# Optimization experiments

Measured on AMD Instinct MI355X. Metric: run time of the kernel, lower is better.

The kernel has to match this reference:

```python
import jax, jax.numpy as jnp
import numpy as np

D_MODEL = 1024
D_INNER = 2048  # expand * d_model
D_STATE = 16
D_CONV = 4
DT_RANK = 64    # ceil(d_model / 16)
B_SZ, L_SEQ = 2, 1024


def setup_inputs() -> dict:
    key = jax.random.key(0)
    ks = jax.random.split(key, 8)
    s = lambda fan_in: 1.0 / np.sqrt(fan_in)
    x = jax.random.normal(ks[0], (B_SZ, L_SEQ, D_MODEL), dtype=jnp.float32)
    in_proj_w = jax.random.normal(ks[1], (2 * D_INNER, D_MODEL), jnp.float32) * s(D_MODEL)
    conv_w = jax.random.normal(ks[2], (D_INNER, 1, D_CONV), jnp.float32) * s(D_CONV)
    conv_b = jax.random.normal(ks[3], (D_INNER,), jnp.float32) * 0.02
    x_proj_w = jax.random.normal(ks[4], (DT_RANK + 2 * D_STATE, D_INNER), jnp.float32) * s(D_INNER)
    dt_proj_w = jax.random.normal(ks[5], (D_INNER, DT_RANK), jnp.float32) * s(DT_RANK)
    dt_proj_b = jax.random.normal(ks[6], (D_INNER,), jnp.float32) * 0.02
    A_log = jnp.broadcast_to(jnp.log(jnp.arange(1, D_STATE + 1, dtype=jnp.float32)), (D_INNER, D_STATE))
    D_param = jnp.ones((D_INNER,), jnp.float32)
    out_proj_w = jax.random.normal(ks[7], (D_MODEL, D_INNER), jnp.float32) * s(D_INNER)
    return dict(x=x, in_proj_w=in_proj_w, conv_w=conv_w, conv_b=conv_b,
                x_proj_w=x_proj_w, dt_proj_w=dt_proj_w, dt_proj_b=dt_proj_b,
                A_log=A_log, D_param=D_param, out_proj_w=out_proj_w)


def _mamba_forward(x, in_proj_w, conv_w, conv_b, x_proj_w, dt_proj_w, dt_proj_b, A_log, D_param, out_proj_w):
    B, L, _ = x.shape
    # in_proj: (B,L,2*d_inner) -> split into conv branch and gate
    xz = jnp.einsum('bld,ed->ble', x, in_proj_w)
    x_br, z = jnp.split(xz, 2, axis=-1)
    # depthwise causal conv1d (left pad d_conv-1, truncate to L == torch pad+slice)
    xc = jnp.transpose(x_br, (0, 2, 1))  # (B, d_inner, L)
    xc = jax.lax.conv_general_dilated(
        xc, conv_w, window_strides=(1,), padding=[(D_CONV - 1, 0)],
        dimension_numbers=('NCH', 'OIH', 'NCH'), feature_group_count=D_INNER)
    xc = xc + conv_b[None, :, None]
    u = jax.nn.silu(jnp.transpose(xc, (0, 2, 1)))  # (B, L, d_inner) = SSM input
    # input-dependent params
    proj = jnp.einsum('bld,ed->ble', u, x_proj_w)
    delta_raw, B_in, C_in = jnp.split(proj, [DT_RANK, DT_RANK + D_STATE], axis=-1)
    delta = jax.nn.softplus(jnp.einsum('blr,dr->bld', delta_raw, dt_proj_w) + dt_proj_b)
    A = -jnp.exp(A_log)  # (d_inner, d_state)

    def step(h, inp):
        d_t, b_t, c_t, u_t = inp  # (B,d_inner),(B,d_state),(B,d_state),(B,d_inner)
        dA = jnp.exp(d_t[:, :, None] * A)                       # (B,d_inner,d_state)
        h = dA * h + (d_t * u_t)[:, :, None] * b_t[:, None, :]  # ZOH-ish update
        y_t = jnp.einsum('bds,bs->bd', h, c_t) + D_param * u_t
        return h, y_t

    h0 = jnp.zeros((B, D_INNER, D_STATE), dtype=x.dtype)
    inputs = (jnp.swapaxes(delta, 0, 1), jnp.swapaxes(B_in, 0, 1),
              jnp.swapaxes(C_in, 0, 1), jnp.swapaxes(u, 0, 1))
    _, ys = jax.lax.scan(step, h0, inputs)  # (L, B, d_inner)
    y = jnp.swapaxes(ys, 0, 1) * jax.nn.silu(z)
    return jnp.einsum('ble,de->bld', y, out_proj_w)


def reference(x, in_proj_w, conv_w, conv_b, x_proj_w, dt_proj_w, dt_proj_b, A_log, D_param, out_proj_w):
    return _mamba_forward(x, in_proj_w, conv_w, conv_b, x_proj_w, dt_proj_w, dt_proj_b, A_log, D_param, out_proj_w)
```

## Files before the change

kernel.cpp:

```cpp
#include <hip/hip_runtime.h>
#include <hip/hip_bf16.h>

#define D_MODEL 1024
#define D_INNER 2048
#define D_STATE 16
#define D_CONV  4
#define DT_RANK 64
#define B_SZ    2
#define L_SEQ   1024
#define BL      (B_SZ * L_SEQ)
#define NPROJ   (DT_RANK + 2 * D_STATE)

typedef __attribute__((ext_vector_type(8))) short bf16x8;
typedef __attribute__((ext_vector_type(4))) float floatx4;
typedef unsigned short ushort_t;

__device__ __forceinline__ void mfma_bf16(floatx4& acc, bf16x8 a, bf16x8 b) {
    asm volatile("v_mfma_f32_16x16x32_bf16 %0, %1, %2, %0"
                 : "+v"(acc) : "v"(a), "v"(b));
}

__device__ __forceinline__ void cvt_hilo(float f, ushort_t& hi, ushort_t& lo) {
    __hip_bfloat16 h = __float2bfloat16(f);
    hi = *(ushort_t*)&h;
    __hip_bfloat16 l = __float2bfloat16(f - __bfloat162float(h));
    lo = *(ushort_t*)&l;
}

__device__ __forceinline__ void cvt_store4(float4 v, ushort_t* hi, ushort_t* lo) {
    ushort4 h, l;
    cvt_hilo(v.x, h.x, l.x);
    cvt_hilo(v.y, h.y, l.y);
    cvt_hilo(v.z, h.z, l.z);
    cvt_hilo(v.w, h.w, l.w);
    *(ushort4*)hi = h;
    *(ushort4*)lo = l;
}

#define N4_WI 1048576
#define N4_WO 524288
#define N4_X  524288
#define N4_WD 32768
#define N4_TOT  (N4_WI + N4_WO + N4_X + N4_WD)

__global__ __launch_bounds__(256) void cvt_static(
    const float* __restrict__ wi, ushort_t* wihi, ushort_t* wilo,
    const float* __restrict__ wo, ushort_t* wohi, ushort_t* wolo,
    const float* __restrict__ x,  ushort_t* xhi,  ushort_t* xlo,
    const float* __restrict__ wd, ushort_t* wdhi, ushort_t* wdlo)
{
    int i = blockIdx.x * 256 + threadIdx.x;
    if (i >= N4_TOT) return;
    const float* src; ushort_t *dh, *dl;
    if (i < N4_WI)                 { src = wi; dh = wihi; dl = wilo; }
    else if ((i -= N4_WI) < N4_WO) { src = wo; dh = wohi; dl = wolo; }
    else if ((i -= N4_WO) < N4_X)  { src = x;  dh = xhi;  dl = xlo;  }
    else                           { i -= N4_X; src = wd; dh = wdhi; dl = wdlo; }
    float4 v = ((const float4*)src)[i];
    cvt_store4(v, dh + i * 4, dl + i * 4);
}

template <int TM, int TN, int KSPLIT, int EPI>
__global__ __launch_bounds__(256, 2) void gemm_pre(
    const ushort_t* __restrict__ Ahi, const ushort_t* __restrict__ Alo, int lda,
    const ushort_t* __restrict__ Bhi, const ushort_t* __restrict__ Blo, int ldb,
    float* __restrict__ C, int ldc, int K, size_t cslice,
    const float* __restrict__ bias)
{
    static_assert(TM == 128 && TN == 128, "stage mapping assumes 128x128");
    constexpr int LDT = 32;
    constexpr int IT = TM / 32, JT = TN / 32;
    __shared__ __align__(16) ushort_t As[2][2][TM * LDT];
    __shared__ __align__(16) ushort_t Bs[2][2][TN * LDT];

    const int tid = threadIdx.x;
    const int bm = blockIdx.y * TM;
    const int bn = blockIdx.x * TN;
    const int kstart = (KSPLIT > 1) ? blockIdx.z * (K / KSPLIT) : 0;
    const int kend   = (KSPLIT > 1) ? kstart + K / KSPLIT : K;

    const int wave = tid >> 6;
    const int lane = tid & 63;
    const int wm = (wave >> 1) * (TM / 2);
    const int wn = (wave & 1) * (TN / 2);
    const int ml = lane & 15;
    const int q  = lane >> 4;

    const ushort_t* gplane = (wave == 0) ? Ahi : (wave == 1) ? Alo
                           : (wave == 2) ? Bhi : Blo;
    const int grow0 = (wave < 2) ? bm : bn;
    const int gld   = (wave < 2) ? lda : ldb;
    const int rsub  = lane >> 2;
    const int gg    = ((lane & 3) ^ ((lane >> 3) & 3)) * 8;

    auto stage = [&](int buf, int kc) {
        ushort_t* lbase = (wave < 2) ? &As[buf][wave & 1][0]
                                     : &Bs[buf][wave & 1][0];
#pragma unroll
        for (int u = 0; u < 8; ++u) {
            const int R0 = u * 16;
            const ushort_t* src =
                gplane + (size_t)(grow0 + R0 + rsub) * gld + kc + gg;
            __builtin_amdgcn_global_load_lds(
                (const __attribute__((address_space(1))) unsigned int*)src,
                (__attribute__((address_space(3))) unsigned int*)(lbase + R0 * LDT),
                16, 0, 0);
        }
    };

    floatx4 acc[IT][JT];
#pragma unroll
    for (int i = 0; i < IT; ++i)
#pragma unroll
        for (int j = 0; j < JT; ++j) acc[i][j] = (floatx4)0.f;

    const int nt = (kend - kstart) >> 5;

    stage(0, kstart);
    __syncthreads();

    for (int t = 0; t < nt; ++t) {
        const int buf = t & 1;
        if (t + 1 < nt) stage(buf ^ 1, kstart + ((t + 1) << 5));

        bf16x8 ah[IT], al[IT], bh[JT], bl[JT];
#pragma unroll
        for (int i = 0; i < IT; ++i) {
            const int r = wm + i * 16 + ml;
            const int p = (q ^ ((r >> 1) & 3)) * 8;
            ah[i] = *(const bf16x8*)&As[buf][0][r * LDT + p];
            al[i] = *(const bf16x8*)&As[buf][1][r * LDT + p];
        }
#pragma unroll
        for (int j = 0; j < JT; ++j) {
            const int r = wn + j * 16 + ml;
            const int p = (q ^ ((r >> 1) & 3)) * 8;
            bh[j] = *(const bf16x8*)&Bs[buf][0][r * LDT + p];
            bl[j] = *(const bf16x8*)&Bs[buf][1][r * LDT + p];
        }
#pragma unroll
        for (int i = 0; i < IT; ++i)
#pragma unroll
            for (int j = 0; j < JT; ++j) {
                mfma_bf16(acc[i][j], ah[i], bh[j]);
                mfma_bf16(acc[i][j], ah[i], bl[j]);
                mfma_bf16(acc[i][j], al[i], bh[j]);
            }

        __syncthreads();
    }

    asm volatile("s_nop 7\n\ts_nop 7\n\ts_nop 7" ::: "memory");

    float* Cb = (KSPLIT > 1) ? C + (size_t)blockIdx.z * cslice : C;
#pragma unroll
    for (int i = 0; i < IT; ++i)
#pragma unroll
        for (int j = 0; j < JT; ++j) {
            const int col = bn + wn + j * 16 + ml;
            const float bv = (EPI == 1) ? bias[col] : 0.f;
#pragma unroll
            for (int r = 0; r < 4; ++r) {
                const int row = bm + wm + i * 16 + q * 4 + r;
                float v = acc[i][j][r];
                if (EPI == 1) {
                    v += bv;
                    v = (v > 20.f) ? v : log1pf(__expf(v));
                }
                Cb[(size_t)row * ldc + col] = v;
            }
        }
}

__global__ __launch_bounds__(256) void fold_out(
    const float* __restrict__ s, float* __restrict__ out)
{
    const int i = blockIdx.x * 256 + threadIdx.x;
    const float4* s4 = (const float4*)s;
    constexpr int SL = BL * D_MODEL / 4;
    float4 a = s4[i], b = s4[i + SL], c = s4[i + 2 * SL], d = s4[i + 3 * SL];
    ((float4*)out)[i] = make_float4(a.x + b.x + c.x + d.x,
                                    a.y + b.y + c.y + d.y,
                                    a.z + b.z + c.z + d.z,
                                    a.w + b.w + c.w + d.w);
}

__global__ __launch_bounds__(256) void fold_proj(
    const float* __restrict__ pp, float* __restrict__ proj,
    ushort_t* __restrict__ Phi, ushort_t* __restrict__ Plo)
{
    const int i = blockIdx.x * 256 + threadIdx.x;
    constexpr int SL = BL * NPROJ / 4;
    float4 acc = make_float4(0.f, 0.f, 0.f, 0.f);
#pragma unroll
    for (int sp = 0; sp < 16; ++sp) {
        float4 v = ((const float4*)pp)[i + sp * SL];
        acc.x += v.x; acc.y += v.y; acc.z += v.z; acc.w += v.w;
    }
    ((float4*)proj)[i] = acc;

    const int row = i / (NPROJ / 4);
    const int c4  = i % (NPROJ / 4);
    if (c4 < DT_RANK / 4)
        cvt_store4(acc, Phi + (size_t)row * DT_RANK + c4 * 4,
                        Plo + (size_t)row * DT_RANK + c4 * 4);
}

#define PKC 128
#define PSC 64

__global__ __launch_bounds__(256) void gemm_proj_conv(
    const float* __restrict__ xz,
    const float* __restrict__ conv_w,
    const float* __restrict__ conv_b,
    const float* __restrict__ Wp,
    float* __restrict__ projp,
    float* __restrict__ u_out)
{
    __shared__ float us[PSC][65];
    __shared__ float wsh[PSC][100];

    const int tid = threadIdx.x;
    const int bm = blockIdx.y * 64;
    const int kbase0 = blockIdx.x * PKC;

    const int tx = tid & 15;
    const int ty = tid >> 4;

    float acc[4][6];
#pragma unroll
    for (int i = 0; i < 4; ++i)
#pragma unroll
        for (int j = 0; j < 6; ++j) acc[i][j] = 0.f;

    for (int sc = 0; sc < PKC / PSC; ++sc) {
        const int kb = kbase0 + sc * PSC;
        __syncthreads();
#pragma unroll
        for (int i = 0; i < 4; ++i) {
            const int flat = tid + 256 * i;
            const int r  = flat >> 4;
            const int kk = (flat & 15) * 4;
            const int k  = kb + kk;
            const int rr = bm + r;
            const int t  = rr & (L_SEQ - 1);
            const float* base = xz + (size_t)rr * 4096 + k;
            float4 x0 = *(const float4*)(base);
            float4 x1 = (t >= 1) ? *(const float4*)(base - 4096)  : make_float4(0,0,0,0);
            float4 x2 = (t >= 2) ? *(const float4*)(base - 8192)  : make_float4(0,0,0,0);
            float4 x3 = (t >= 3) ? *(const float4*)(base - 12288) : make_float4(0,0,0,0);
            float4 cb = *(const float4*)(conv_b + k);
            float4 w0 = ((const float4*)conv_w)[k + 0];
            float4 w1 = ((const float4*)conv_w)[k + 1];
            float4 w2 = ((const float4*)conv_w)[k + 2];
            float4 w3 = ((const float4*)conv_w)[k + 3];
            float4 uo;
            { float a = cb.x + w0.x*x3.x + w0.y*x2.x + w0.z*x1.x + w0.w*x0.x;
              uo.x = a / (1.f + __expf(-a)); }
            { float a = cb.y + w1.x*x3.y + w1.y*x2.y + w1.z*x1.y + w1.w*x0.y;
              uo.y = a / (1.f + __expf(-a)); }
            { float a = cb.z + w2.x*x3.z + w2.y*x2.z + w2.z*x1.z + w2.w*x0.z;
              uo.z = a / (1.f + __expf(-a)); }
            { float a = cb.w + w3.x*x3.w + w3.y*x2.w + w3.z*x1.w + w3.w*x0.w;
              uo.w = a / (1.f + __expf(-a)); }
            us[kk + 0][r] = uo.x;
            us[kk + 1][r] = uo.y;
            us[kk + 2][r] = uo.z;
            us[kk + 3][r] = uo.w;
            *(float4*)(u_out + (size_t)rr * D_INNER + k) = uo;
        }
#pragma unroll
        for (int i = 0; i < 6; ++i) {
            const int flat = tid + 256 * i;
            const int r = flat >> 4;
            const int k4 = flat & 15;
            float4 v = *(const float4*)(Wp + (size_t)r * D_INNER + kb + k4 * 4);
            wsh[k4*4+0][r] = v.x; wsh[k4*4+1][r] = v.y;
            wsh[k4*4+2][r] = v.z; wsh[k4*4+3][r] = v.w;
        }
        __syncthreads();

#pragma unroll 8
        for (int kk = 0; kk < PSC; ++kk) {
            float a[4], b[6];
#pragma unroll
            for (int i = 0; i < 4; ++i) a[i] = us[kk][ty * 4 + i];
#pragma unroll
            for (int j = 0; j < 6; ++j) b[j] = wsh[kk][tx + 16 * j];
#pragma unroll
            for (int i = 0; i < 4; ++i)
#pragma unroll
                for (int j = 0; j < 6; ++j) acc[i][j] += a[i] * b[j];
        }
    }

    float* pb = projp + (size_t)blockIdx.x * (BL * NPROJ);
#pragma unroll
    for (int i = 0; i < 4; ++i)
#pragma unroll
        for (int j = 0; j < 6; ++j)
            pb[(size_t)(bm + ty * 4 + i) * NPROJ + tx + 16 * j] = acc[i][j];
}

template <int CSv>
__global__ __launch_bounds__(256) void scan_phase_a(
    const float* __restrict__ xz,
    const float* __restrict__ u,
    const float* __restrict__ proj,
    const float* __restrict__ A_log,
    float* __restrict__ hloc,
    float* __restrict__ sumd,
    int nc)
{
    const int d = blockIdx.x * 256 + threadIdx.x;
    const int c = blockIdx.y;
    const int b = blockIdx.z;

    float a[D_STATE];
#pragma unroll
    for (int s = 0; s < D_STATE; ++s) a[s] = -__expf(A_log[d * D_STATE + s]);

    float h[D_STATE];
#pragma unroll
    for (int s = 0; s < D_STATE; ++s) h[s] = 0.f;
    float sd = 0.f;

    for (int t = c * CSv; t < (c + 1) * CSv; ++t) {
        const size_t bt = (size_t)b * L_SEQ + t;
        const float dv = xz[bt * (2 * D_INNER) + d];
        const float uv = u[bt * D_INNER + d];
        const float du = dv * uv;
        sd += dv;
        const float* pr = proj + bt * NPROJ;
#pragma unroll
        for (int s = 0; s < D_STATE; ++s)
            h[s] = __expf(dv * a[s]) * h[s] + du * pr[DT_RANK + s];
    }

    const size_t base = ((size_t)(b * nc + c) * D_STATE) * D_INNER + d;
#pragma unroll
    for (int s = 0; s < D_STATE; ++s) hloc[base + (size_t)s * D_INNER] = h[s];
    sumd[(size_t)(b * nc + c) * D_INNER + d] = sd;
}

__global__ __launch_bounds__(256) void scan_phase_b(
    const float* __restrict__ hloc,
    const float* __restrict__ sumd,
    const float* __restrict__ A_log,
    float* __restrict__ carry,
    int nc)
{
    const int g = blockIdx.x * 256 + threadIdx.x;
    const int d = g & (D_INNER - 1);
    const int s = (g >> 11) & (D_STATE - 1);
    const int b = g >> 15;

    const float a_s = -__expf(A_log[d * D_STATE + s]);

    float hc = 0.f;
    carry[((size_t)(b * nc + 0) * D_STATE + s) * D_INNER + d] = 0.f;

    for (int c = 1; c < nc; ++c) {
        const float sd = sumd[(size_t)(b * nc + c - 1) * D_INNER + d];
        const float hl = hloc[((size_t)(b * nc + c - 1) * D_STATE + s) * D_INNER + d];
        hc = __expf(a_s * sd) * hc + hl;
        carry[((size_t)(b * nc + c) * D_STATE + s) * D_INNER + d] = hc;
    }
}

template <int CSv>
__global__ __launch_bounds__(256) void scan_phase_c(
    const float* __restrict__ xz,
    const float* __restrict__ u,
    const float* __restrict__ proj,
    const float* __restrict__ A_log,
    const float* __restrict__ D_param,
    const float* __restrict__ carry,
    ushort_t* __restrict__ Yhi,
    ushort_t* __restrict__ Ylo,
    int nc)
{
    const int d = blockIdx.x * 256 + threadIdx.x;
    const int c = blockIdx.y;
    const int b = blockIdx.z;

    float a[D_STATE];
#pragma unroll
    for (int s = 0; s < D_STATE; ++s) a[s] = -__expf(A_log[d * D_STATE + s]);
    const float Dp = D_param[d];

    float h[D_STATE];
    const size_t cbase = ((size_t)(b * nc + c) * D_STATE) * D_INNER + d;
#pragma unroll
    for (int s = 0; s < D_STATE; ++s) h[s] = carry[cbase + (size_t)s * D_INNER];

    for (int t = c * CSv; t < (c + 1) * CSv; ++t) {
        const size_t bt = (size_t)b * L_SEQ + t;
        const float dv = xz[bt * (2 * D_INNER) + d];
        const float uv = u[bt * D_INNER + d];
        const float du = dv * uv;
        const float* pr = proj + bt * NPROJ;

        float acc = 0.f;
#pragma unroll
        for (int s = 0; s < D_STATE; ++s) {
            h[s] = __expf(dv * a[s]) * h[s] + du * pr[DT_RANK + s];
            acc += h[s] * pr[DT_RANK + D_STATE + s];
        }
        const float yv = acc + Dp * uv;

        const float zv = xz[bt * (2 * D_INNER) + D_INNER + d];
        const float gate = zv / (1.f + __expf(-zv));
        ushort_t hh, ll;
        cvt_hilo(yv * gate, hh, ll);
        Yhi[bt * D_INNER + d] = hh;
        Ylo[bt * D_INNER + d] = ll;
    }
}

extern "C" void kernel_launch(void* const* d_in, const int* in_sizes, int n_in,
                              void* d_out, int out_size, void* d_ws, size_t ws_size,
                              hipStream_t stream)
{
    const float* x         = (const float*)d_in[0];
    const float* in_proj_w = (const float*)d_in[1];
    const float* conv_w    = (const float*)d_in[2];
    const float* conv_b    = (const float*)d_in[3];
    const float* x_proj_w  = (const float*)d_in[4];
    const float* dt_proj_w = (const float*)d_in[5];
    const float* dt_proj_b = (const float*)d_in[6];
    const float* A_log     = (const float*)d_in[7];
    const float* D_param   = (const float*)d_in[8];
    const float* out_proj_w= (const float*)d_in[9];
    float* out = (float*)d_out;

    const size_t fixed =
        (size_t)BL * 4096 * 4 +
        (size_t)BL * 2048 * 4 +
        (size_t)BL * NPROJ * 4 +
        (size_t)(4096 + 2048) * 1024 * 2 * 2;
    const size_t need64 = fixed + (size_t)B_SZ * 64 * D_INNER * 4
                                + (size_t)B_SZ * 64 * D_STATE * D_INNER * 4;
    const int nc = (ws_size >= need64) ? 64 : 32;
    const int cs = L_SEQ / nc;

    float* xz    = (float*)d_ws;
    float* u     = xz    + (size_t)BL * 4096;
    float* proj  = u     + (size_t)BL * 2048;
    float* sumd  = proj  + (size_t)BL * NPROJ;
    float* carry = sumd  + (size_t)B_SZ * nc * D_INNER;
    ushort_t* Wihi = (ushort_t*)(carry + (size_t)B_SZ * nc * D_STATE * D_INNER);
    ushort_t* Wilo = Wihi + (size_t)4096 * 1024;
    ushort_t* Wohi = Wilo + (size_t)4096 * 1024;
    ushort_t* Wolo = Wohi + (size_t)1024 * 2048;
    ushort_t* Xhi  = (ushort_t*)carry;
    ushort_t* Xlo  = Xhi + (size_t)BL * D_MODEL;
    float*    hloc = (float*)Wihi;
    ushort_t* Yhi  = Wihi;
    ushort_t* Ylo  = Wilo;
    float*    projp = (float*)Wihi;
    ushort_t* Phi  = Xhi;
    ushort_t* Plo  = Xhi + (size_t)BL * DT_RANK;
    ushort_t* Wdhi = (ushort_t*)sumd;
    ushort_t* Wdlo = Wdhi + (size_t)D_INNER * DT_RANK;
    float*    Cslc  = xz;

    dim3 blk(256);

    cvt_static<<<(N4_TOT + 255) / 256, blk, 0, stream>>>(
        in_proj_w, Wihi, Wilo, out_proj_w, Wohi, Wolo, x, Xhi, Xlo,
        dt_proj_w, Wdhi, Wdlo);

    gemm_pre<128, 128, 1, 0><<<dim3(4096 / 128, BL / 128), blk, 0, stream>>>(
        Xhi, Xlo, D_MODEL, Wihi, Wilo, D_MODEL, xz, 2 * D_INNER, D_MODEL, 0,
        nullptr);

    gemm_proj_conv<<<dim3(D_INNER / PKC, BL / 64), blk, 0, stream>>>(
        xz, conv_w, conv_b, x_proj_w, projp, u);

    fold_proj<<<(BL * NPROJ / 4) / 256, blk, 0, stream>>>(projp, proj, Phi, Plo);

    gemm_pre<128, 128, 1, 1><<<dim3(D_INNER / 128, BL / 128), blk, 0, stream>>>(
        Phi, Plo, DT_RANK, Wdhi, Wdlo, DT_RANK, xz, 2 * D_INNER, DT_RANK, 0,
        dt_proj_b);

    if (cs == 16) {
        scan_phase_a<16><<<dim3(D_INNER / 256, nc, B_SZ), blk, 0, stream>>>(
            xz, u, proj, A_log, hloc, sumd, nc);
    } else {
        scan_phase_a<32><<<dim3(D_INNER / 256, nc, B_SZ), blk, 0, stream>>>(
            xz, u, proj, A_log, hloc, sumd, nc);
    }
    scan_phase_b<<<dim3((B_SZ * D_INNER * D_STATE) / 256), blk, 0, stream>>>(
        hloc, sumd, A_log, carry, nc);
    if (cs == 16) {
        scan_phase_c<16><<<dim3(D_INNER / 256, nc, B_SZ), blk, 0, stream>>>(
            xz, u, proj, A_log, D_param, carry, Yhi, Ylo, nc);
    } else {
        scan_phase_c<32><<<dim3(D_INNER / 256, nc, B_SZ), blk, 0, stream>>>(
            xz, u, proj, A_log, D_param, carry, Yhi, Ylo, nc);
    }

    gemm_pre<128, 128, 4, 0><<<dim3(D_MODEL / 128, BL / 128, 4), blk, 0, stream>>>(
        Yhi, Ylo, D_INNER, Wohi, Wolo, D_INNER, Cslc, D_MODEL, D_INNER,
        (size_t)BL * D_MODEL, nullptr);
    fold_out<<<(BL * D_MODEL / 4) / 256, blk, 0, stream>>>(Cslc, out);
}
```

Baseline: 302.0 us.

## Add 512-thread 128x256 triple-buffered GEMM for in_proj and out_proj

Introduces a gemm_big kernel with 8 waves, a 128x256 output tile and a three-stage LDS ring. Six waves issue direct global-to-LDS loads and synchronisation uses vmcnt waits plus a raw s_barrier, so loads run two tiles ahead of compute. The in_proj and split-K out_proj GEMMs now use it, while gemm_pre keeps only the dt_proj path. The larger tile raises per-block data reuse and the deeper pipeline hides load latency, but it costs more LDS and registers (one block per CU) and leaves fewer blocks in each grid.

```diff
diff --git a/kernel.cpp b/kernel.cpp
--- a/kernel.cpp
+++ b/kernel.cpp
@@ -60,11 +60,120 @@
     cvt_store4(v, dh + i * 4, dl + i * 4);
 }
 
-template <int TM, int TN, int KSPLIT, int EPI>
+template <int KSPLIT>
+__global__ __launch_bounds__(512, 1) void gemm_big(
+    const ushort_t* __restrict__ Ahi, const ushort_t* __restrict__ Alo, int lda,
+    const ushort_t* __restrict__ Bhi, const ushort_t* __restrict__ Blo, int ldb,
+    float* __restrict__ C, int ldc, int K, size_t cslice)
+{
+    constexpr int BM = 128, BN = 256, LDT = 32;
+    __shared__ __align__(16) ushort_t As[3][2][BM * LDT];
+    __shared__ __align__(16) ushort_t Bs[3][2][BN * LDT];
+
+    const int tid = threadIdx.x;
+    const int bm = blockIdx.y * BM;
+    const int bn = blockIdx.x * BN;
+    const int kstart = (KSPLIT > 1) ? blockIdx.z * (K / KSPLIT) : 0;
+    const int nt = ((KSPLIT > 1) ? K / KSPLIT : K) >> 5;
+
+    const int wave = tid >> 6;
+    const int lane = tid & 63;
+    const int wm = (wave >> 2) * 64;
+    const int wn = (wave & 3) * 64;
+    const int ml = lane & 15;
+    const int q  = lane >> 4;
+
+    const int rsub = lane >> 2;
+    const int gg   = ((lane & 3) ^ ((lane >> 3) & 3)) * 8;
+    const ushort_t* gsrc = Ahi; int grow0 = bm, gld = lda;
+    if (wave == 1)      { gsrc = Alo; grow0 = bm;       gld = lda; }
+    else if (wave == 2) { gsrc = Bhi; grow0 = bn;       gld = ldb; }
+    else if (wave == 3) { gsrc = Bhi; grow0 = bn + 128; gld = ldb; }
+    else if (wave == 4) { gsrc = Blo; grow0 = bn;       gld = ldb; }
+    else if (wave == 5) { gsrc = Blo; grow0 = bn + 128; gld = ldb; }
+    const bool do_stage = (wave < 6);
+
+    auto stage = [&](int buf, int kc) {
+        if (!do_stage) return;
+        ushort_t* lb;
+        if (wave == 0)      lb = &As[buf][0][0];
+        else if (wave == 1) lb = &As[buf][1][0];
+        else if (wave == 2) lb = &Bs[buf][0][0];
+        else if (wave == 3) lb = &Bs[buf][0][128 * LDT];
+        else if (wave == 4) lb = &Bs[buf][1][0];
+        else                lb = &Bs[buf][1][128 * LDT];
+#pragma unroll
+        for (int u2 = 0; u2 < 8; ++u2) {
+            const int R0 = u2 * 16;
+            const ushort_t* src =
+                gsrc + (size_t)(grow0 + R0 + rsub) * gld + kc + gg;
+            __builtin_amdgcn_global_load_lds(
+                (const __attribute__((address_space(1))) unsigned int*)src,
+                (__attribute__((address_space(3))) unsigned int*)(lb + R0 * LDT),
+                16, 0, 0);
+        }
+    };
+
+    floatx4 acc[4][4];
+#pragma unroll
+    for (int i = 0; i < 4; ++i)
+#pragma unroll
+        for (int j = 0; j < 4; ++j) acc[i][j] = (floatx4)0.f;
+
+    stage(0, kstart);
+    if (nt > 1) stage(1, kstart + 32);
+
+    for (int t = 0; t < nt; ++t) {
+        asm volatile("s_waitcnt vmcnt(8)" ::: "memory");
+        __builtin_amdgcn_s_barrier();
+        if (t + 2 < nt) stage((t + 2) % 3, kstart + ((t + 2) << 5));
+
+        const int buf = t % 3;
+        bf16x8 ah[4], al[4], bh[4], bl[4];
+#pragma unroll
+        for (int i = 0; i < 4; ++i) {
+            const int r = wm + i * 16 + ml;
+            const int p = (q ^ ((r >> 1) & 3)) * 8;
+            ah[i] = *(const bf16x8*)&As[buf][0][r * LDT + p];
+            al[i] = *(const bf16x8*)&As[buf][1][r * LDT + p];
+        }
+#pragma unroll
+        for (int j = 0; j < 4; ++j) {
+            const int r = wn + j * 16 + ml;
+            const int p = (q ^ ((r >> 1) & 3)) * 8;
+            bh[j] = *(const bf16x8*)&Bs[buf][0][r * LDT + p];
+            bl[j] = *(const bf16x8*)&Bs[buf][1][r * LDT + p];
+        }
+#pragma unroll
+        for (int i = 0; i < 4; ++i)
+#pragma unroll
+            for (int j = 0; j < 4; ++j) {
+                mfma_bf16(acc[i][j], ah[i], bh[j]);
+                mfma_bf16(acc[i][j], ah[i], bl[j]);
+                mfma_bf16(acc[i][j], al[i], bh[j]);
+            }
+    }
+
+    asm volatile("s_nop 7\n\ts_nop 7\n\ts_nop 7" ::: "memory");
+
+    float* Cb = (KSPLIT > 1) ? C + (size_t)blockIdx.z * cslice : C;
+#pragma unroll
+    for (int i = 0; i < 4; ++i)
+#pragma unroll
+        for (int j = 0; j < 4; ++j)
+#pragma unroll
+            for (int r = 0; r < 4; ++r) {
+                const int row = bm + wm + i * 16 + q * 4 + r;
+                const int col = bn + wn + j * 16 + ml;
+                Cb[(size_t)row * ldc + col] = acc[i][j][r];
+            }
+}
+
+template <int TM, int TN, int EPI>
 __global__ __launch_bounds__(256, 2) void gemm_pre(
     const ushort_t* __restrict__ Ahi, const ushort_t* __restrict__ Alo, int lda,
     const ushort_t* __restrict__ Bhi, const ushort_t* __restrict__ Blo, int ldb,
-    float* __restrict__ C, int ldc, int K, size_t cslice,
+    float* __restrict__ C, int ldc, int K,
     const float* __restrict__ bias)
 {
     static_assert(TM == 128 && TN == 128, "stage mapping assumes 128x128");
@@ -76,8 +185,6 @@
     const int tid = threadIdx.x;
     const int bm = blockIdx.y * TM;
     const int bn = blockIdx.x * TN;
-    const int kstart = (KSPLIT > 1) ? blockIdx.z * (K / KSPLIT) : 0;
-    const int kend   = (KSPLIT > 1) ? kstart + K / KSPLIT : K;
 
     const int wave = tid >> 6;
     const int lane = tid & 63;
@@ -114,14 +221,14 @@
 #pragma unroll
         for (int j = 0; j < JT; ++j) acc[i][j] = (floatx4)0.f;
 
-    const int nt = (kend - kstart) >> 5;
-
-    stage(0, kstart);
+    const int nt = K >> 5;
+
+    stage(0, 0);
     __syncthreads();
 
     for (int t = 0; t < nt; ++t) {
         const int buf = t & 1;
-        if (t + 1 < nt) stage(buf ^ 1, kstart + ((t + 1) << 5));
+        if (t + 1 < nt) stage(buf ^ 1, (t + 1) << 5);
 
         bf16x8 ah[IT], al[IT], bh[JT], bl[JT];
 #pragma unroll
@@ -152,7 +259,6 @@
 
     asm volatile("s_nop 7\n\ts_nop 7\n\ts_nop 7" ::: "memory");
 
-    float* Cb = (KSPLIT > 1) ? C + (size_t)blockIdx.z * cslice : C;
 #pragma unroll
     for (int i = 0; i < IT; ++i)
 #pragma unroll
@@ -167,7 +273,7 @@
                     v += bv;
                     v = (v > 20.f) ? v : log1pf(__expf(v));
                 }
-                Cb[(size_t)row * ldc + col] = v;
+                C[(size_t)row * ldc + col] = v;
             }
         }
 }
@@ -466,22 +572,22 @@
     float*    Cslc  = xz;
 
     dim3 blk(256);
+    dim3 blk512(512);
 
     cvt_static<<<(N4_TOT + 255) / 256, blk, 0, stream>>>(
         in_proj_w, Wihi, Wilo, out_proj_w, Wohi, Wolo, x, Xhi, Xlo,
         dt_proj_w, Wdhi, Wdlo);
 
-    gemm_pre<128, 128, 1, 0><<<dim3(4096 / 128, BL / 128), blk, 0, stream>>>(
-        Xhi, Xlo, D_MODEL, Wihi, Wilo, D_MODEL, xz, 2 * D_INNER, D_MODEL, 0,
-        nullptr);
+    gemm_big<1><<<dim3(4096 / 256, BL / 128), blk512, 0, stream>>>(
+        Xhi, Xlo, D_MODEL, Wihi, Wilo, D_MODEL, xz, 2 * D_INNER, D_MODEL, 0);
 
     gemm_proj_conv<<<dim3(D_INNER / PKC, BL / 64), blk, 0, stream>>>(
         xz, conv_w, conv_b, x_proj_w, projp, u);
 
     fold_proj<<<(BL * NPROJ / 4) / 256, blk, 0, stream>>>(projp, proj, Phi, Plo);
 
-    gemm_pre<128, 128, 1, 1><<<dim3(D_INNER / 128, BL / 128), blk, 0, stream>>>(
-        Phi, Plo, DT_RANK, Wdhi, Wdlo, DT_RANK, xz, 2 * D_INNER, DT_RANK, 0,
+    gemm_pre<128, 128, 1><<<dim3(D_INNER / 128, BL / 128), blk, 0, stream>>>(
+        Phi, Plo, DT_RANK, Wdhi, Wdlo, DT_RANK, xz, 2 * D_INNER, DT_RANK,
         dt_proj_b);
 
     if (cs == 16) {
@@ -501,8 +607,8 @@
             xz, u, proj, A_log, D_param, carry, Yhi, Ylo, nc);
     }
 
-    gemm_pre<128, 128, 4, 0><<<dim3(D_MODEL / 128, BL / 128, 4), blk, 0, stream>>>(
+    gemm_big<4><<<dim3(D_MODEL / 256, BL / 128, 4), blk512, 0, stream>>>(
         Yhi, Ylo, D_INNER, Wohi, Wolo, D_INNER, Cslc, D_MODEL, D_INNER,
-        (size_t)BL * D_MODEL, nullptr);
+        (size_t)BL * D_MODEL);
     fold_out<<<(BL * D_MODEL / 4) / 256, blk, 0, stream>>>(Cslc, out);
 }
```

Result: faster. 295.0 us (-2.3%).
